# Performance work log

Hardware: AMD Instinct MI355X
Metric: run time of the kernel (lower is better)

The kernel has to match this reference:

```python
import jax, jax.numpy as jnp
import numpy as np

B, SQ, SK = 4, 4096, 1024
HID, SATD = 640, 768
NUM_HEADS, HEAD_DIM = 10, 64
GEO_RATIO, ROPE_BASE = 1.0, 10000.0
LOSS_W = 0.05


def _ln(x, g, b):
    m = x.mean(-1, keepdims=True)
    v = ((x - m) ** 2).mean(-1, keepdims=True)
    return (x - m) / jnp.sqrt(v + 1e-5) * g + b


def _rope(t, xy):
    # t: [B,H,S,D], xy: [B,S,2] continuous coordinates.
    # Half the rotary channels encode x, half encode y.
    q = HEAD_DIM // 4
    inv = ROPE_BASE ** (-jnp.arange(q, dtype=t.dtype) / q)  # [q]
    ang = jnp.concatenate([xy[..., 0:1] * GEO_RATIO * inv,
                           xy[..., 1:2] * GEO_RATIO * inv], axis=-1)  # [B,S,D/2]
    cos = jnp.cos(ang)[:, None]  # [B,1,S,D/2]
    sin = jnp.sin(ang)[:, None]
    t1, t2 = t[..., : HEAD_DIM // 2], t[..., HEAD_DIM // 2:]
    return jnp.concatenate([t1 * cos - t2 * sin, t1 * sin + t2 * cos], axis=-1)


def setup_inputs() -> dict:
    key = jax.random.key(0)
    ks = jax.random.split(key, 16)
    s = 0.02
    return {
        'hidden_states': jax.random.normal(ks[0], (B, SQ, HID), jnp.float32),
        'sat_tokens': jax.random.normal(ks[1], (B, SK, SATD), jnp.float32),
        'sat_xy': jax.random.normal(ks[2], (B, SK, 2), jnp.float32) * 10.0,
        'front_bev_xy': jax.random.normal(ks[3], (B, SQ, 2), jnp.float32) * 10.0,
        'front_plucker': jax.random.normal(ks[4], (B, SQ, 6), jnp.float32),
        'valid_mask': jax.random.uniform(ks[5], (B, SQ), jnp.float32),
        'Wq': jax.random.normal(ks[6], (HID, HID), jnp.float32) * s,
        'bq': jnp.zeros((HID,), jnp.float32),
        'sat_ln_g': jnp.ones((SATD,), jnp.float32),
        'sat_ln_b': jnp.zeros((SATD,), jnp.float32),
        'Wk': jax.random.normal(ks[7], (SATD, HID), jnp.float32) * s,
        'bk': jnp.zeros((HID,), jnp.float32),
        'Wv': jax.random.normal(ks[8], (SATD, HID), jnp.float32) * s,
        'bv': jnp.zeros((HID,), jnp.float32),
        'Wp1': jax.random.normal(ks[9], (6, HID), jnp.float32) * s,
        'bp1': jnp.zeros((HID,), jnp.float32),
        'Wp2': jax.random.normal(ks[10], (HID, HID), jnp.float32) * s,
        'bp2': jnp.zeros((HID,), jnp.float32),
        'gate_ln_g': jnp.ones((HID,), jnp.float32),
        'gate_ln_b': jnp.zeros((HID,), jnp.float32),
        'Wg': jax.random.normal(ks[11], (HID, 1), jnp.float32) * s,
        'bg': jnp.full((1,), -1.0, jnp.float32),
    }


def reference(hidden_states, sat_tokens, sat_xy, front_bev_xy, front_plucker,
              valid_mask, Wq, bq, sat_ln_g, sat_ln_b, Wk, bk, Wv, bv,
              Wp1, bp1, Wp2, bp2, gate_ln_g, gate_ln_b, Wg, bg):
    b = hidden_states.shape[0]
    sn = _ln(sat_tokens, sat_ln_g, sat_ln_b)
    query = hidden_states @ Wq + bq                      # [B,SQ,HID]
    key = sn @ Wk + bk                                   # [B,SK,HID]
    value = sn @ Wv + bv
    q = query.reshape(b, -1, NUM_HEADS, HEAD_DIM).transpose(0, 2, 1, 3)
    k = key.reshape(b, -1, NUM_HEADS, HEAD_DIM).transpose(0, 2, 1, 3)
    v = value.reshape(b, -1, NUM_HEADS, HEAD_DIM).transpose(0, 2, 1, 3)
    q = _rope(q, front_bev_xy)
    k = _rope(k, sat_xy)
    logits = jnp.einsum('bhqd,bhkd->bhqk', q, k) / np.sqrt(HEAD_DIM)
    probs = jax.nn.softmax(logits.astype(jnp.float32), axis=-1).astype(q.dtype)
    out_h = jnp.einsum('bhqk,bhkd->bhqd', probs, v)
    out_h = out_h.transpose(0, 2, 1, 3).reshape(b, -1, HID)
    # plucker-conditioned gate
    pf = jax.nn.silu(front_plucker @ Wp1 + bp1) @ Wp2 + bp2
    gate_ctx = hidden_states + pf
    gate = jax.nn.sigmoid(_ln(gate_ctx, gate_ln_g, gate_ln_b) @ Wg + bg)  # [B,SQ,1]
    vm = (valid_mask > 0.5)
    out = out_h * gate * vm[..., None].astype(out_h.dtype)
    # auxiliary masked-mean confidence loss over invalid positions
    inv = (~vm).astype(gate.dtype)
    denom = jnp.maximum(inv.sum(), 1.0)
    loss = (gate[..., 0] * inv).sum() / denom * LOSS_W
    return out, loss
```

## Files before the change

kernel.cpp:

```cpp
#include <hip/hip_runtime.h>
#include <cstdint>
#include <cstddef>

#define B_    4
#define SQ_   4096
#define SK_   1024
#define HID_  640
#define SATD_ 768
#define NH_   10
#define HD_   64

typedef __bf16 bf16_t;
typedef __bf16 bf16x4 __attribute__((ext_vector_type(4)));
typedef __bf16 bf16x8 __attribute__((ext_vector_type(8)));
typedef float  f32x4  __attribute__((ext_vector_type(4)));
typedef unsigned short u16x8 __attribute__((ext_vector_type(8)));

static __device__ __forceinline__ unsigned short f2u(float f) {
  bf16_t b = (bf16_t)f;
  return __builtin_bit_cast(unsigned short, b);
}
static __device__ __forceinline__ float u2f(unsigned short u) {
  return (float)__builtin_bit_cast(bf16_t, u);
}
static __device__ __forceinline__ f32x4 mfma16(bf16x8 a, bf16x8 b, f32x4 c) {
  return __builtin_amdgcn_mfma_f32_16x16x32_bf16(a, b, c, 0, 0, 0);
}
static __device__ __forceinline__ void glds16(const unsigned short* g, unsigned short* l) {
  __builtin_amdgcn_global_load_lds((const __attribute__((address_space(1))) void*)g,
                                   (__attribute__((address_space(3))) void*)l, 16, 0, 0);
}

__global__ __launch_bounds__(256) void k_transpose4(const float* __restrict__ Wq,
                                                    const float* __restrict__ Wk,
                                                    const float* __restrict__ Wv,
                                                    const float* __restrict__ Wp2,
                                                    unsigned short* __restrict__ wqT,
                                                    unsigned short* __restrict__ kvT,
                                                    unsigned short* __restrict__ wp2T) {
  __shared__ unsigned short tile[64 * 65];
  int seg = blockIdx.y;
  const float* W; unsigned short* D; int K;
  if (seg == 0)      { W = Wq;  D = wqT;  K = 640; }
  else if (seg == 1) { W = Wk;  D = kvT;  K = 768; }
  else if (seg == 2) { W = Wv;  D = kvT + (size_t)640 * 768; K = 768; }
  else               { W = Wp2; D = wp2T; K = 640; }
  const int ktiles = K / 64;
  int kt = blockIdx.x % ktiles, ntile = blockIdx.x / ktiles;
  if (ntile >= 10) return;
  const int k0 = kt * 64, n0 = ntile * 64;
  const int t = threadIdx.x, r = t >> 3, c8 = (t & 7) * 8;
#pragma unroll
  for (int i = 0; i < 2; i++) {
    int row = r + i * 32;
    const float* wp = W + (size_t)(k0 + row) * HID_ + n0 + c8;
    float4 a0 = *(const float4*)wp, a1 = *(const float4*)(wp + 4);
    tile[(c8 + 0) * 65 + row] = f2u(a0.x);
    tile[(c8 + 1) * 65 + row] = f2u(a0.y);
    tile[(c8 + 2) * 65 + row] = f2u(a0.z);
    tile[(c8 + 3) * 65 + row] = f2u(a0.w);
    tile[(c8 + 4) * 65 + row] = f2u(a1.x);
    tile[(c8 + 5) * 65 + row] = f2u(a1.y);
    tile[(c8 + 6) * 65 + row] = f2u(a1.z);
    tile[(c8 + 7) * 65 + row] = f2u(a1.w);
  }
  __syncthreads();
#pragma unroll
  for (int i = 0; i < 2; i++) {
    int nl = r + i * 32;
    u16x8 o;
#pragma unroll
    for (int u = 0; u < 8; u++) o[u] = tile[nl * 65 + c8 + u];
    *(u16x8*)(D + (size_t)(n0 + nl) * K + k0 + c8) = o;
  }
}

__global__ void k_concat_bias(const float* __restrict__ bk, const float* __restrict__ bv,
                              float* __restrict__ out) {
  int i = blockIdx.x * 256 + threadIdx.x;
  if (i < HID_) out[i] = bk[i];
  else if (i < 2 * HID_) out[i] = bv[i - HID_];
}

__global__ __launch_bounds__(256) void k_satln(const float* __restrict__ x,
                                               const float* __restrict__ g,
                                               const float* __restrict__ bta,
                                               unsigned short* __restrict__ out) {
  int r = blockIdx.x;
  const float* xr = x + (size_t)r * SATD_;
  int t = threadIdx.x;
  float v0 = xr[t], v1 = xr[t + 256], v2 = xr[t + 512];
  float s = v0 + v1 + v2;
  float ss = v0 * v0 + v1 * v1 + v2 * v2;
  __shared__ float sb[8];
  for (int o = 32; o; o >>= 1) { s += __shfl_xor(s, o); ss += __shfl_xor(ss, o); }
  if ((t & 63) == 0) { sb[t >> 6] = s; sb[4 + (t >> 6)] = ss; }
  __syncthreads();
  s  = sb[0] + sb[1] + sb[2] + sb[3];
  ss = sb[4] + sb[5] + sb[6] + sb[7];
  float m = s * (1.f / SATD_);
  float rstd = rsqrtf(ss * (1.f / SATD_) - m * m + 1e-5f);
  unsigned short* orow = out + (size_t)r * SATD_;
  orow[t]       = f2u((v0 - m) * rstd * g[t]       + bta[t]);
  orow[t + 256] = f2u((v1 - m) * rstd * g[t + 256] + bta[t + 256]);
  orow[t + 512] = f2u((v2 - m) * rstd * g[t + 512] + bta[t + 512]);
}

__global__ __launch_bounds__(256) void k_pf1(const float* __restrict__ plk,
                                             const float* __restrict__ W,
                                             const float* __restrict__ bias,
                                             unsigned short* __restrict__ out) {
  int i = blockIdx.x * 256 + threadIdx.x;
  int r = i / 80, c8 = (i - r * 80) * 8;
  const float* p = plk + (size_t)r * 6;
  float pv[6];
#pragma unroll
  for (int j = 0; j < 6; j++) pv[j] = p[j];
  u16x8 o;
#pragma unroll
  for (int u = 0; u < 8; u++) {
    int c = c8 + u;
    float a = bias[c];
#pragma unroll
    for (int j = 0; j < 6; j++) a += pv[j] * W[j * HID_ + c];
    o[u] = f2u(a / (1.f + __expf(-a)));
  }
  *(u16x8*)&out[(size_t)r * HID_ + c8] = o;
}

__global__ __launch_bounds__(256) void k_gemm_fused(const unsigned short* __restrict__ pf1,
                                                    const float* __restrict__ hidden,
                                                    const unsigned short* __restrict__ wp2T,
                                                    const unsigned short* __restrict__ wqT,
                                                    const float* __restrict__ bp2,
                                                    const float* __restrict__ bq,
                                                    unsigned short* __restrict__ pf2,
                                                    unsigned short* __restrict__ q_lin,
                                                    const float* __restrict__ bev_xy) {
  __shared__ unsigned short As[2][128 * 32];
  __shared__ unsigned short Bs[2][128 * 32];
  const int z = blockIdx.z;
  const int bx = blockIdx.x;
  const int xcd = bx & 7, jj = bx >> 3;
  const int bm = ((jj / 5) * 8 + xcd) * 128;
  const int bn = (jj % 5) * 128;
  const int K = 640, N = 640;
  const unsigned short* BT = z ? wqT : wp2T;
  const float* bias = z ? bq : bp2;
  unsigned short* C = z ? q_lin : pf2;

  const int t = threadIdx.x, wv = t >> 6, lane = t & 63;
  const int lc = lane & 15, quad = lane >> 4;
  const int wm = (wv >> 1) * 64, wn = (wv & 1) * 64;
  f32x4 acc[4][4];
  f32x4 zero = {0.f, 0.f, 0.f, 0.f};
#pragma unroll
  for (int i = 0; i < 4; i++)
#pragma unroll
    for (int j = 0; j < 4; j++) acc[i][j] = zero;
  const int srow = wv * 32 + (lane >> 2);
  const int sc8 = (lane & 3) * 8;

  for (int k0 = 0; k0 < K; k0 += 64) {
    __syncthreads();
    if (z == 0) {
#pragma unroll
      for (int h2 = 0; h2 < 2; h2++)
#pragma unroll
        for (int i = 0; i < 2; i++)
          glds16(pf1 + (size_t)(bm + srow + i * 16) * K + k0 + h2 * 32 + sc8,
                 &As[h2][(wv * 32 + i * 16) * 32]);
    } else {
      const int r4 = t >> 2, c4 = (t & 3) * 8;
#pragma unroll
      for (int h2 = 0; h2 < 2; h2++)
#pragma unroll
        for (int i = 0; i < 2; i++) {
          const float* ap = hidden + (size_t)(bm + r4 + i * 64) * K + k0 + h2 * 32 + c4;
          float4 a0 = *(const float4*)ap, a1 = *(const float4*)(ap + 4);
          u16x8 u = { f2u(a0.x), f2u(a0.y), f2u(a0.z), f2u(a0.w),
                      f2u(a1.x), f2u(a1.y), f2u(a1.z), f2u(a1.w) };
          *(u16x8*)&As[h2][(r4 + i * 64) * 32 + c4] = u;
        }
    }
#pragma unroll
    for (int h2 = 0; h2 < 2; h2++)
#pragma unroll
      for (int i = 0; i < 2; i++)
        glds16(BT + (size_t)(bn + srow + i * 16) * K + k0 + h2 * 32 + sc8,
               &Bs[h2][(wv * 32 + i * 16) * 32]);
    __syncthreads();
#pragma unroll
    for (int h2 = 0; h2 < 2; h2++) {
      bf16x8 af[4], bfr[4];
#pragma unroll
      for (int mt = 0; mt < 4; mt++) af[mt]  = *(const bf16x8*)&As[h2][(wm + mt * 16 + lc) * 32 + quad * 8];
#pragma unroll
      for (int nt = 0; nt < 4; nt++) bfr[nt] = *(const bf16x8*)&Bs[h2][(wn + nt * 16 + lc) * 32 + quad * 8];
#pragma unroll
      for (int mt = 0; mt < 4; mt++)
#pragma unroll
        for (int nt = 0; nt < 4; nt++) acc[mt][nt] = mfma16(af[mt], bfr[nt], acc[mt][nt]);
    }
  }

  float bsv[4];
#pragma unroll
  for (int nt = 0; nt < 4; nt++) bsv[nt] = bias[bn + wn + nt * 16 + lc];
  const float inv = __builtin_amdgcn_exp2f(-(float)lc * 0.8304820237218407f);
  const float qscale = 0.18033688011112042f;

#pragma unroll
  for (int mt = 0; mt < 4; mt++) {
    int row = bm + wm + mt * 16 + quad * 4;
#pragma unroll
    for (int r = 0; r < 4; r++) {
      unsigned short* crow = C + (size_t)(row + r) * N + bn + wn + lc;
      float v0 = acc[mt][0][r] + bsv[0];
      float v1 = acc[mt][1][r] + bsv[1];
      float v2 = acc[mt][2][r] + bsv[2];
      float v3 = acc[mt][3][r] + bsv[3];
      if (z) {
        float2 xy = *(const float2*)&bev_xy[(size_t)(row + r) * 2];
        float s0, c0, s1, c1;
        __sincosf(xy.x * inv, &s0, &c0);
        __sincosf(xy.y * inv, &s1, &c1);
        float n0 = (v0 * c0 - v2 * s0) * qscale;
        float n2 = (v0 * s0 + v2 * c0) * qscale;
        float n1 = (v1 * c1 - v3 * s1) * qscale;
        float n3 = (v1 * s1 + v3 * c1) * qscale;
        v0 = n0; v1 = n1; v2 = n2; v3 = n3;
      }
      crow[0]  = f2u(v0);
      crow[16] = f2u(v1);
      crow[32] = f2u(v2);
      crow[48] = f2u(v3);
    }
  }
}

__global__ __launch_bounds__(256) void k_gemm_kv(const unsigned short* __restrict__ sn,
                                                 const unsigned short* __restrict__ kvT,
                                                 const float* __restrict__ bias_kv,
                                                 unsigned short* __restrict__ k_lin,
                                                 unsigned short* __restrict__ vT,
                                                 const float* __restrict__ sat_xy) {
  __shared__ unsigned short As[2][128 * 32];
  __shared__ unsigned short Bs[2][128 * 32];
  const int bx = blockIdx.x;
  const int xcd = bx & 7, jj = bx >> 3;
  const int bm = ((jj / 10) * 8 + xcd) * 128;
  const int bn = (jj % 10) * 128;
  const int K = 768;
  const int t = threadIdx.x, wv = t >> 6, lane = t & 63;
  const int lc = lane & 15, quad = lane >> 4;
  const int wm = (wv >> 1) * 64, wn = (wv & 1) * 64;
  f32x4 acc[4][4];
  f32x4 zero = {0.f, 0.f, 0.f, 0.f};
#pragma unroll
  for (int i = 0; i < 4; i++)
#pragma unroll
    for (int j = 0; j < 4; j++) acc[i][j] = zero;
  const int srow = wv * 32 + (lane >> 2);
  const int sc8 = (lane & 3) * 8;

  for (int k0 = 0; k0 < K; k0 += 64) {
    __syncthreads();
#pragma unroll
    for (int h2 = 0; h2 < 2; h2++)
#pragma unroll
      for (int i = 0; i < 2; i++) {
        glds16(sn  + (size_t)(bm + srow + i * 16) * K + k0 + h2 * 32 + sc8,
               &As[h2][(wv * 32 + i * 16) * 32]);
        glds16(kvT + (size_t)(bn + srow + i * 16) * K + k0 + h2 * 32 + sc8,
               &Bs[h2][(wv * 32 + i * 16) * 32]);
      }
    __syncthreads();
#pragma unroll
    for (int h2 = 0; h2 < 2; h2++) {
      bf16x8 af[4], bfr[4];
#pragma unroll
      for (int mt = 0; mt < 4; mt++) af[mt]  = *(const bf16x8*)&As[h2][(wm + mt * 16 + lc) * 32 + quad * 8];
#pragma unroll
      for (int nt = 0; nt < 4; nt++) bfr[nt] = *(const bf16x8*)&Bs[h2][(wn + nt * 16 + lc) * 32 + quad * 8];
#pragma unroll
      for (int mt = 0; mt < 4; mt++)
#pragma unroll
        for (int nt = 0; nt < 4; nt++) acc[mt][nt] = mfma16(af[mt], bfr[nt], acc[mt][nt]);
    }
  }

  float bsv[4];
#pragma unroll
  for (int nt = 0; nt < 4; nt++) bsv[nt] = bias_kv[bn + wn + nt * 16 + lc];
  const bool isV = (bn >= HID_);
  const float inv = __builtin_amdgcn_exp2f(-(float)lc * 0.8304820237218407f);

  if (!isV) {
#pragma unroll
    for (int mt = 0; mt < 4; mt++) {
      int row = bm + wm + mt * 16 + quad * 4;
#pragma unroll
      for (int r = 0; r < 4; r++) {
        unsigned short* crow = k_lin + (size_t)(row + r) * HID_ + bn + wn + lc;
        float v0 = acc[mt][0][r] + bsv[0];
        float v1 = acc[mt][1][r] + bsv[1];
        float v2 = acc[mt][2][r] + bsv[2];
        float v3 = acc[mt][3][r] + bsv[3];
        float2 xy = *(const float2*)&sat_xy[(size_t)(row + r) * 2];
        float s0, c0, s1, c1;
        __sincosf(xy.x * inv, &s0, &c0);
        __sincosf(xy.y * inv, &s1, &c1);
        crow[0]  = f2u(v0 * c0 - v2 * s0);
        crow[32] = f2u(v0 * s0 + v2 * c0);
        crow[16] = f2u(v1 * c1 - v3 * s1);
        crow[48] = f2u(v1 * s1 + v3 * c1);
      }
    }
  } else {
#pragma unroll
    for (int mt = 0; mt < 4; mt++) {
      int row0 = bm + wm + mt * 16 + quad * 4;
      int bidx = row0 >> 10, key0 = row0 & 1023;
#pragma unroll
      for (int nt = 0; nt < 4; nt++) {
        int d = bn - HID_ + wn + nt * 16 + lc;
        bf16x4 v;
#pragma unroll
        for (int r = 0; r < 4; r++) v[r] = (bf16_t)(acc[mt][nt][r] + bsv[nt]);
        *(bf16x4*)(vT + ((size_t)(bidx * HID_ + d) << 10) + key0) = v;
      }
    }
  }
}

__global__ __launch_bounds__(256) void k_gate(const float* __restrict__ hid,
                                              const unsigned short* __restrict__ pf2,
                                              const float* __restrict__ g,
                                              const float* __restrict__ be,
                                              const float* __restrict__ Wg,
                                              const float* __restrict__ bg,
                                              const float* __restrict__ vm,
                                              float* __restrict__ gate_buf,
                                              float* __restrict__ lg_buf) {
  int r = blockIdx.x;
  const float* hr = hid + (size_t)r * HID_;
  const unsigned short* pr = pf2 + (size_t)r * HID_;
  int t = threadIdx.x;
  __shared__ float xb[HID_];
  __shared__ float sb[8];
  float s = 0.f, ss = 0.f;
  for (int c = t; c < HID_; c += 256) {
    float x = hr[c] + u2f(pr[c]);
    xb[c] = x; s += x; ss += x * x;
  }
  for (int o = 32; o; o >>= 1) { s += __shfl_xor(s, o); ss += __shfl_xor(ss, o); }
  if ((t & 63) == 0) { sb[t >> 6] = s; sb[4 + (t >> 6)] = ss; }
  __syncthreads();
  s  = sb[0] + sb[1] + sb[2] + sb[3];
  ss = sb[4] + sb[5] + sb[6] + sb[7];
  float m = s * (1.f / HID_);
  float rstd = rsqrtf(ss * (1.f / HID_) - m * m + 1e-5f);
  float dacc = 0.f;
  for (int c = t; c < HID_; c += 256)
    dacc += ((xb[c] - m) * rstd * g[c] + be[c]) * Wg[c];
  for (int o = 32; o; o >>= 1) dacc += __shfl_xor(dacc, o);
  __syncthreads();
  if ((t & 63) == 0) sb[t >> 6] = dacc;
  __syncthreads();
  if (t == 0) {
    float dsum = sb[0] + sb[1] + sb[2] + sb[3] + bg[0];
    float gate = 1.f / (1.f + __expf(-dsum));
    float v = vm[r];
    gate_buf[r] = (v > 0.5f) ? gate : 0.f;
    lg_buf[r]   = (v > 0.5f) ? 0.f : gate;
  }
}

__global__ __launch_bounds__(256) void k_attn(const unsigned short* __restrict__ q_lin,
                                              const unsigned short* __restrict__ k_lin,
                                              const unsigned short* __restrict__ vT,
                                              const float* __restrict__ gate_buf,
                                              float* __restrict__ out) {
  __shared__ unsigned short Ks[64 * 72];
  __shared__ unsigned short Vt[64 * 72];
  __shared__ unsigned short Pt[4][32 * 72];
  const int qb = blockIdx.x * 128;
  const int bh = blockIdx.y;
  const int b = bh / NH_, h = bh - b * NH_;
  const int t = threadIdx.x, wv = t >> 6, lane = t & 63;
  const int lc = lane & 15, quad = lane >> 4;
  unsigned short* myPt = &Pt[wv][0];

  const unsigned short* qbase = q_lin + (size_t)(b * SQ_ + qb + wv * 32 + lc) * HID_ + h * HD_;
  bf16x8 qf[2][2];
#pragma unroll
  for (int g = 0; g < 2; g++) {
    qf[g][0] = *(const bf16x8*)(qbase + (size_t)g * 16 * HID_ + quad * 8);
    qf[g][1] = *(const bf16x8*)(qbase + (size_t)g * 16 * HID_ + 32 + quad * 8);
  }
  f32x4 zero = {0.f, 0.f, 0.f, 0.f};
  f32x4 O[2][4];
#pragma unroll
  for (int g = 0; g < 2; g++)
#pragma unroll
    for (int dt = 0; dt < 4; dt++) O[g][dt] = zero;
  float l_run[2] = {0.f, 0.f};

  const unsigned short* Kg = k_lin + (size_t)b * SK_ * HID_ + h * HD_;
  const unsigned short* Vg = vT + ((size_t)b * HID_ + h * HD_) * SK_;
  const int srow = t >> 3, scol = (t & 7) * 8;

  for (int kc = 0; kc < SK_; kc += 64) {
    __syncthreads();
#pragma unroll
    for (int i = 0; i < 2; i++) {
      int row = srow + i * 32;
      *(u16x8*)&Ks[row * 72 + scol] = *(const u16x8*)(Kg + (size_t)(kc + row) * HID_ + scol);
      *(u16x8*)&Vt[row * 72 + scol] = *(const u16x8*)(Vg + (size_t)row * SK_ + kc + scol);
    }
    __syncthreads();

    f32x4 ST[2][4];
#pragma unroll
    for (int kt = 0; kt < 4; kt++) {
      bf16x8 ka0 = *(const bf16x8*)&Ks[(kt * 16 + lc) * 72 + quad * 8];
      bf16x8 ka1 = *(const bf16x8*)&Ks[(kt * 16 + lc) * 72 + 32 + quad * 8];
#pragma unroll
      for (int g = 0; g < 2; g++)
        ST[g][kt] = mfma16(ka1, qf[g][1], mfma16(ka0, qf[g][0], zero));
    }
#pragma unroll
    for (int g = 0; g < 2; g++) {
      float rs = 0.f;
#pragma unroll
      for (int kt = 0; kt < 4; kt++) {
        bf16x4 pk;
#pragma unroll
        for (int r = 0; r < 4; r++) {
          float p = __builtin_amdgcn_exp2f(ST[g][kt][r]);
          rs += p;
          pk[r] = (bf16_t)p;
        }
        *(bf16x4*)&myPt[(g * 16 + lc) * 72 + kt * 16 + quad * 4] = pk;
      }
      rs += __shfl_xor(rs, 16);
      rs += __shfl_xor(rs, 32);
      l_run[g] += rs;
    }
#pragma unroll
    for (int ks = 0; ks < 2; ks++) {
      bf16x8 va[4];
#pragma unroll
      for (int dt = 0; dt < 4; dt++)
        va[dt] = *(const bf16x8*)&Vt[(dt * 16 + lc) * 72 + ks * 32 + quad * 8];
#pragma unroll
      for (int g = 0; g < 2; g++) {
        bf16x8 pb = *(const bf16x8*)&myPt[(g * 16 + lc) * 72 + ks * 32 + quad * 8];
#pragma unroll
        for (int dt = 0; dt < 4; dt++)
          O[g][dt] = mfma16(va[dt], pb, O[g][dt]);
      }
    }
  }

#pragma unroll
  for (int g = 0; g < 2; g++) {
    int rg = b * SQ_ + qb + wv * 32 + g * 16 + lc;
    float gv = gate_buf[rg] / l_run[g];
    float* orow = out + (size_t)rg * HID_ + h * HD_;
#pragma unroll
    for (int dt = 0; dt < 4; dt++) {
      f32x4 o4 = O[g][dt] * gv;
      *(f32x4*)&orow[dt * 16 + quad * 4] = o4;
    }
  }
}

__global__ __launch_bounds__(256) void k_loss(const float* __restrict__ lg,
                                              const float* __restrict__ vm,
                                              float* __restrict__ out_loss) {
  int t = threadIdx.x;
  float s = 0.f, cnt = 0.f;
  for (int i = t; i < B_ * SQ_; i += 256) {
    s += lg[i];
    cnt += (vm[i] > 0.5f) ? 0.f : 1.f;
  }
  __shared__ float sb[8];
  for (int o = 32; o; o >>= 1) { s += __shfl_xor(s, o); cnt += __shfl_xor(cnt, o); }
  if ((t & 63) == 0) { sb[t >> 6] = s; sb[4 + (t >> 6)] = cnt; }
  __syncthreads();
  if (t == 0) {
    s   = sb[0] + sb[1] + sb[2] + sb[3];
    cnt = sb[4] + sb[5] + sb[6] + sb[7];
    out_loss[0] = s / fmaxf(cnt, 1.f) * 0.05f;
  }
}

extern "C" void kernel_launch(void* const* d_in, const int* in_sizes, int n_in,
                              void* d_out, int out_size, void* d_ws, size_t ws_size,
                              hipStream_t stream) {
  (void)in_sizes; (void)n_in; (void)out_size; (void)ws_size;
  const float* hidden = (const float*)d_in[0];
  const float* sat    = (const float*)d_in[1];
  const float* sat_xy = (const float*)d_in[2];
  const float* bev_xy = (const float*)d_in[3];
  const float* plk    = (const float*)d_in[4];
  const float* vm     = (const float*)d_in[5];
  const float* Wq     = (const float*)d_in[6];
  const float* bq     = (const float*)d_in[7];
  const float* slg    = (const float*)d_in[8];
  const float* slb    = (const float*)d_in[9];
  const float* Wk     = (const float*)d_in[10];
  const float* bk     = (const float*)d_in[11];
  const float* Wv     = (const float*)d_in[12];
  const float* bv     = (const float*)d_in[13];
  const float* Wp1    = (const float*)d_in[14];
  const float* bp1    = (const float*)d_in[15];
  const float* Wp2    = (const float*)d_in[16];
  const float* bp2    = (const float*)d_in[17];
  const float* glg    = (const float*)d_in[18];
  const float* glb    = (const float*)d_in[19];
  const float* Wg     = (const float*)d_in[20];
  const float* bg     = (const float*)d_in[21];
  float* out = (float*)d_out;

  char* ws = (char*)d_ws;
  size_t off = 0;
  auto alloc = [&](size_t bytes) -> char* {
    char* p = ws + off;
    off += (bytes + 255) & ~(size_t)255;
    return p;
  };
  char* regP = alloc((size_t)16384 * 640 * 2);
  unsigned short* pf1   = (unsigned short*)regP;
  unsigned short* k_lin = (unsigned short*)regP;
  unsigned short* vT    = (unsigned short*)(regP + (size_t)4096 * 640 * 2);
  unsigned short* pf2   = (unsigned short*)alloc((size_t)16384 * 640 * 2);
  unsigned short* q_lin = (unsigned short*)alloc((size_t)16384 * 640 * 2);
  unsigned short* sn    = (unsigned short*)alloc((size_t)4096 * 768 * 2);
  unsigned short* wqT   = (unsigned short*)alloc((size_t)640 * 640 * 2);
  unsigned short* kvT   = (unsigned short*)alloc((size_t)1280 * 768 * 2);
  unsigned short* wp2T  = (unsigned short*)alloc((size_t)640 * 640 * 2);
  float* bias_kv  = (float*)alloc(1280 * 4);
  float* gate_buf = (float*)alloc(16384 * 4);
  float* lg_buf   = (float*)alloc(16384 * 4);

  {
    dim3 g(120, 4);
    k_transpose4<<<g, 256, 0, stream>>>(Wq, Wk, Wv, Wp2, wqT, kvT, wp2T);
  }
  k_concat_bias<<<5, 256, 0, stream>>>(bk, bv, bias_kv);

  k_pf1<<<16384 * 80 / 256, 256, 0, stream>>>(plk, Wp1, bp1, pf1);
  k_satln<<<4096, 256, 0, stream>>>(sat, slg, slb, sn);

  {
    dim3 g(640, 1, 2);
    k_gemm_fused<<<g, 256, 0, stream>>>(pf1, hidden, wp2T, wqT, bp2, bq, pf2, q_lin, bev_xy);
  }
  k_gemm_kv<<<320, 256, 0, stream>>>(sn, kvT, bias_kv, k_lin, vT, sat_xy);

  k_gate<<<16384, 256, 0, stream>>>(hidden, pf2, glg, glb, Wg, bg, vm, gate_buf, lg_buf);

  {
    dim3 g(SQ_ / 128, B_ * NH_);
    k_attn<<<g, 256, 0, stream>>>(q_lin, k_lin, vT, gate_buf, out);
  }
  k_loss<<<1, 256, 0, stream>>>(lg_buf, vm, out + (size_t)B_ * SQ_ * HID_);
}
```

Before: 354.3 us.

## Merge prep kernels, fuse KV GEMM into batched GEMM, warp-per-row gate, prefetch attn tiles

Folds the weight transpose, bias concat, satellite LayerNorm and plucker MLP first layer into one launch, and runs the K/V projection as a third z-slice of the Q/pf2 GEMM kernel. The gate kernel now handles one row per wavefront, which removes shared-memory reductions and block barriers. The attention kernel prefetches the next K/V chunk into registers while computing on the current one. pf2 is stored in the output buffer as scratch, and the workspace regions are no longer aliased. The aim is to cut launch overhead and idle tails and to overlap global loads with compute, at the cost of higher register pressure in attention.

New measurement: 309.1 us. 1.15x faster.

```diff
diff --git a/kernel.cpp b/kernel.cpp
--- a/kernel.cpp
+++ b/kernel.cpp
@@ -31,123 +31,140 @@
                                    (__attribute__((address_space(3))) void*)l, 16, 0, 0);
 }
 
-__global__ __launch_bounds__(256) void k_transpose4(const float* __restrict__ Wq,
-                                                    const float* __restrict__ Wk,
-                                                    const float* __restrict__ Wv,
-                                                    const float* __restrict__ Wp2,
-                                                    unsigned short* __restrict__ wqT,
-                                                    unsigned short* __restrict__ kvT,
-                                                    unsigned short* __restrict__ wp2T) {
+__global__ __launch_bounds__(256) void k_prep(const float* __restrict__ Wq,
+                                              const float* __restrict__ Wk,
+                                              const float* __restrict__ Wv,
+                                              const float* __restrict__ Wp2,
+                                              unsigned short* __restrict__ wqT,
+                                              unsigned short* __restrict__ kvT,
+                                              unsigned short* __restrict__ wp2T,
+                                              const float* __restrict__ bk,
+                                              const float* __restrict__ bv,
+                                              float* __restrict__ bias_kv,
+                                              const float* __restrict__ sat,
+                                              const float* __restrict__ slg,
+                                              const float* __restrict__ slb,
+                                              unsigned short* __restrict__ sn,
+                                              const float* __restrict__ plk,
+                                              const float* __restrict__ Wp1,
+                                              const float* __restrict__ bp1,
+                                              unsigned short* __restrict__ pf1) {
   __shared__ unsigned short tile[64 * 65];
-  int seg = blockIdx.y;
-  const float* W; unsigned short* D; int K;
-  if (seg == 0)      { W = Wq;  D = wqT;  K = 640; }
-  else if (seg == 1) { W = Wk;  D = kvT;  K = 768; }
-  else if (seg == 2) { W = Wv;  D = kvT + (size_t)640 * 768; K = 768; }
-  else               { W = Wp2; D = wp2T; K = 640; }
-  const int ktiles = K / 64;
-  int kt = blockIdx.x % ktiles, ntile = blockIdx.x / ktiles;
-  if (ntile >= 10) return;
-  const int k0 = kt * 64, n0 = ntile * 64;
-  const int t = threadIdx.x, r = t >> 3, c8 = (t & 7) * 8;
-#pragma unroll
-  for (int i = 0; i < 2; i++) {
-    int row = r + i * 32;
-    const float* wp = W + (size_t)(k0 + row) * HID_ + n0 + c8;
-    float4 a0 = *(const float4*)wp, a1 = *(const float4*)(wp + 4);
-    tile[(c8 + 0) * 65 + row] = f2u(a0.x);
-    tile[(c8 + 1) * 65 + row] = f2u(a0.y);
-    tile[(c8 + 2) * 65 + row] = f2u(a0.z);
-    tile[(c8 + 3) * 65 + row] = f2u(a0.w);
-    tile[(c8 + 4) * 65 + row] = f2u(a1.x);
-    tile[(c8 + 5) * 65 + row] = f2u(a1.y);
-    tile[(c8 + 6) * 65 + row] = f2u(a1.z);
-    tile[(c8 + 7) * 65 + row] = f2u(a1.w);
-  }
-  __syncthreads();
-#pragma unroll
-  for (int i = 0; i < 2; i++) {
-    int nl = r + i * 32;
+  __shared__ float sb[8];
+  const int bx = blockIdx.x, t = threadIdx.x;
+
+  if (bx < 480) {
+    int seg = bx / 120, inner = bx % 120;
+    const float* W; unsigned short* D; int K;
+    if (seg == 0)      { W = Wq;  D = wqT;  K = 640; }
+    else if (seg == 1) { W = Wk;  D = kvT;  K = 768; }
+    else if (seg == 2) { W = Wv;  D = kvT + (size_t)640 * 768; K = 768; }
+    else               { W = Wp2; D = wp2T; K = 640; }
+    const int ktiles = K / 64;
+    int kt = inner % ktiles, ntile = inner / ktiles;
+    if (ntile >= 10) return;
+    const int k0 = kt * 64, n0 = ntile * 64;
+    const int r = t >> 3, c8 = (t & 7) * 8;
+#pragma unroll
+    for (int i = 0; i < 2; i++) {
+      int row = r + i * 32;
+      const float* wp = W + (size_t)(k0 + row) * HID_ + n0 + c8;
+      float4 a0 = *(const float4*)wp, a1 = *(const float4*)(wp + 4);
+      tile[(c8 + 0) * 65 + row] = f2u(a0.x);
+      tile[(c8 + 1) * 65 + row] = f2u(a0.y);
+      tile[(c8 + 2) * 65 + row] = f2u(a0.z);
+      tile[(c8 + 3) * 65 + row] = f2u(a0.w);
+      tile[(c8 + 4) * 65 + row] = f2u(a1.x);
+      tile[(c8 + 5) * 65 + row] = f2u(a1.y);
+      tile[(c8 + 6) * 65 + row] = f2u(a1.z);
+      tile[(c8 + 7) * 65 + row] = f2u(a1.w);
+    }
+    __syncthreads();
+#pragma unroll
+    for (int i = 0; i < 2; i++) {
+      int nl = r + i * 32;
+      u16x8 o;
+#pragma unroll
+      for (int u = 0; u < 8; u++) o[u] = tile[nl * 65 + c8 + u];
+      *(u16x8*)(D + (size_t)(n0 + nl) * K + k0 + c8) = o;
+    }
+  } else if (bx < 485) {
+    int i = (bx - 480) * 256 + t;
+    if (i < HID_) bias_kv[i] = bk[i];
+    else if (i < 2 * HID_) bias_kv[i] = bv[i - HID_];
+  } else if (bx < 4581) {
+    int r = bx - 485;
+    const float* xr = sat + (size_t)r * SATD_;
+    float v0 = xr[t], v1 = xr[t + 256], v2 = xr[t + 512];
+    float s = v0 + v1 + v2;
+    float ss = v0 * v0 + v1 * v1 + v2 * v2;
+    for (int o = 32; o; o >>= 1) { s += __shfl_xor(s, o); ss += __shfl_xor(ss, o); }
+    if ((t & 63) == 0) { sb[t >> 6] = s; sb[4 + (t >> 6)] = ss; }
+    __syncthreads();
+    s  = sb[0] + sb[1] + sb[2] + sb[3];
+    ss = sb[4] + sb[5] + sb[6] + sb[7];
+    float m = s * (1.f / SATD_);
+    float rstd = rsqrtf(ss * (1.f / SATD_) - m * m + 1e-5f);
+    unsigned short* orow = sn + (size_t)r * SATD_;
+    orow[t]       = f2u((v0 - m) * rstd * slg[t]       + slb[t]);
+    orow[t + 256] = f2u((v1 - m) * rstd * slg[t + 256] + slb[t + 256]);
+    orow[t + 512] = f2u((v2 - m) * rstd * slg[t + 512] + slb[t + 512]);
+  } else {
+    int i = (bx - 4581) * 256 + t;
+    int r = i / 80, c8 = (i - r * 80) * 8;
+    const float* p = plk + (size_t)r * 6;
+    float pv[6];
+#pragma unroll
+    for (int j = 0; j < 6; j++) pv[j] = p[j];
     u16x8 o;
 #pragma unroll
-    for (int u = 0; u < 8; u++) o[u] = tile[nl * 65 + c8 + u];
-    *(u16x8*)(D + (size_t)(n0 + nl) * K + k0 + c8) = o;
-  }
-}
-
-__global__ void k_concat_bias(const float* __restrict__ bk, const float* __restrict__ bv,
-                              float* __restrict__ out) {
-  int i = blockIdx.x * 256 + threadIdx.x;
-  if (i < HID_) out[i] = bk[i];
-  else if (i < 2 * HID_) out[i] = bv[i - HID_];
-}
-
-__global__ __launch_bounds__(256) void k_satln(const float* __restrict__ x,
-                                               const float* __restrict__ g,
-                                               const float* __restrict__ bta,
-                                               unsigned short* __restrict__ out) {
-  int r = blockIdx.x;
-  const float* xr = x + (size_t)r * SATD_;
-  int t = threadIdx.x;
-  float v0 = xr[t], v1 = xr[t + 256], v2 = xr[t + 512];
-  float s = v0 + v1 + v2;
-  float ss = v0 * v0 + v1 * v1 + v2 * v2;
-  __shared__ float sb[8];
-  for (int o = 32; o; o >>= 1) { s += __shfl_xor(s, o); ss += __shfl_xor(ss, o); }
-  if ((t & 63) == 0) { sb[t >> 6] = s; sb[4 + (t >> 6)] = ss; }
-  __syncthreads();
-  s  = sb[0] + sb[1] + sb[2] + sb[3];
-  ss = sb[4] + sb[5] + sb[6] + sb[7];
-  float m = s * (1.f / SATD_);
-  float rstd = rsqrtf(ss * (1.f / SATD_) - m * m + 1e-5f);
-  unsigned short* orow = out + (size_t)r * SATD_;
-  orow[t]       = f2u((v0 - m) * rstd * g[t]       + bta[t]);
-  orow[t + 256] = f2u((v1 - m) * rstd * g[t + 256] + bta[t + 256]);
-  orow[t + 512] = f2u((v2 - m) * rstd * g[t + 512] + bta[t + 512]);
-}
-
-__global__ __launch_bounds__(256) void k_pf1(const float* __restrict__ plk,
-                                             const float* __restrict__ W,
-                                             const float* __restrict__ bias,
-                                             unsigned short* __restrict__ out) {
-  int i = blockIdx.x * 256 + threadIdx.x;
-  int r = i / 80, c8 = (i - r * 80) * 8;
-  const float* p = plk + (size_t)r * 6;
-  float pv[6];
-#pragma unroll
-  for (int j = 0; j < 6; j++) pv[j] = p[j];
-  u16x8 o;
-#pragma unroll
-  for (int u = 0; u < 8; u++) {
-    int c = c8 + u;
-    float a = bias[c];
-#pragma unroll
-    for (int j = 0; j < 6; j++) a += pv[j] * W[j * HID_ + c];
-    o[u] = f2u(a / (1.f + __expf(-a)));
-  }
-  *(u16x8*)&out[(size_t)r * HID_ + c8] = o;
-}
-
-__global__ __launch_bounds__(256) void k_gemm_fused(const unsigned short* __restrict__ pf1,
-                                                    const float* __restrict__ hidden,
-                                                    const unsigned short* __restrict__ wp2T,
-                                                    const unsigned short* __restrict__ wqT,
-                                                    const float* __restrict__ bp2,
-                                                    const float* __restrict__ bq,
-                                                    unsigned short* __restrict__ pf2,
-                                                    unsigned short* __restrict__ q_lin,
-                                                    const float* __restrict__ bev_xy) {
+    for (int u = 0; u < 8; u++) {
+      int c = c8 + u;
+      float a = bp1[c];
+#pragma unroll
+      for (int j = 0; j < 6; j++) a += pv[j] * Wp1[j * HID_ + c];
+      o[u] = f2u(a / (1.f + __expf(-a)));
+    }
+    *(u16x8*)&pf1[(size_t)r * HID_ + c8] = o;
+  }
+}
+
+__global__ __launch_bounds__(256) void k_gemm3(const unsigned short* __restrict__ pf1,
+                                               const float* __restrict__ hidden,
+                                               const unsigned short* __restrict__ sn,
+                                               const unsigned short* __restrict__ wp2T,
+                                               const unsigned short* __restrict__ wqT,
+                                               const unsigned short* __restrict__ kvT,
+                                               const float* __restrict__ bp2,
+                                               const float* __restrict__ bq,
+                                               const float* __restrict__ bias_kv,
+                                               unsigned short* __restrict__ pf2,
+                                               unsigned short* __restrict__ q_lin,
+                                               unsigned short* __restrict__ k_lin,
+                                               unsigned short* __restrict__ vT,
+                                               const float* __restrict__ bev_xy,
+                                               const float* __restrict__ sat_xy) {
   __shared__ unsigned short As[2][128 * 32];
   __shared__ unsigned short Bs[2][128 * 32];
   const int z = blockIdx.z;
   const int bx = blockIdx.x;
-  const int xcd = bx & 7, jj = bx >> 3;
-  const int bm = ((jj / 5) * 8 + xcd) * 128;
-  const int bn = (jj % 5) * 128;
-  const int K = 640, N = 640;
-  const unsigned short* BT = z ? wqT : wp2T;
-  const float* bias = z ? bq : bp2;
-  unsigned short* C = z ? q_lin : pf2;
+  int bm, bn, K;
+  const unsigned short* BT;
+  const float* bias;
+  if (z == 2) {
+    if (bx >= 320) return;
+    const int xcd = bx & 7, jj = bx >> 3;
+    bm = ((jj / 10) * 8 + xcd) * 128;
+    bn = (jj % 10) * 128;
+    K = 768; BT = kvT; bias = bias_kv;
+  } else {
+    const int xcd = bx & 7, jj = bx >> 3;
+    bm = ((jj / 5) * 8 + xcd) * 128;
+    bn = (jj % 5) * 128;
+    K = 640;
+    BT = z ? wqT : wp2T;
+    bias = z ? bq : bp2;
+  }
 
   const int t = threadIdx.x, wv = t >> 6, lane = t & 63;
   const int lc = lane & 15, quad = lane >> 4;
@@ -169,6 +186,13 @@
 #pragma unroll
         for (int i = 0; i < 2; i++)
           glds16(pf1 + (size_t)(bm + srow + i * 16) * K + k0 + h2 * 32 + sc8,
+                 &As[h2][(wv * 32 + i * 16) * 32]);
+    } else if (z == 2) {
+#pragma unroll
+      for (int h2 = 0; h2 < 2; h2++)
+#pragma unroll
+        for (int i = 0; i < 2; i++)
+          glds16(sn + (size_t)(bm + srow + i * 16) * K + k0 + h2 * 32 + sc8,
                  &As[h2][(wv * 32 + i * 16) * 32]);
     } else {
       const int r4 = t >> 2, c4 = (t & 3) * 8;
@@ -208,95 +232,43 @@
 #pragma unroll
   for (int nt = 0; nt < 4; nt++) bsv[nt] = bias[bn + wn + nt * 16 + lc];
   const float inv = __builtin_amdgcn_exp2f(-(float)lc * 0.8304820237218407f);
-  const float qscale = 0.18033688011112042f;
-
-#pragma unroll
-  for (int mt = 0; mt < 4; mt++) {
-    int row = bm + wm + mt * 16 + quad * 4;
-#pragma unroll
-    for (int r = 0; r < 4; r++) {
-      unsigned short* crow = C + (size_t)(row + r) * N + bn + wn + lc;
-      float v0 = acc[mt][0][r] + bsv[0];
-      float v1 = acc[mt][1][r] + bsv[1];
-      float v2 = acc[mt][2][r] + bsv[2];
-      float v3 = acc[mt][3][r] + bsv[3];
-      if (z) {
+
+  if (z == 0) {
+#pragma unroll
+    for (int mt = 0; mt < 4; mt++) {
+      int row = bm + wm + mt * 16 + quad * 4;
+#pragma unroll
+      for (int r = 0; r < 4; r++) {
+        unsigned short* crow = pf2 + (size_t)(row + r) * HID_ + bn + wn + lc;
+        crow[0]  = f2u(acc[mt][0][r] + bsv[0]);
+        crow[16] = f2u(acc[mt][1][r] + bsv[1]);
+        crow[32] = f2u(acc[mt][2][r] + bsv[2]);
+        crow[48] = f2u(acc[mt][3][r] + bsv[3]);
+      }
+    }
+  } else if (z == 1) {
+    const float qscale = 0.18033688011112042f;
+#pragma unroll
+    for (int mt = 0; mt < 4; mt++) {
+      int row = bm + wm + mt * 16 + quad * 4;
+#pragma unroll
+      for (int r = 0; r < 4; r++) {
+        unsigned short* crow = q_lin + (size_t)(row + r) * HID_ + bn + wn + lc;
+        float v0 = acc[mt][0][r] + bsv[0];
+        float v1 = acc[mt][1][r] + bsv[1];
+        float v2 = acc[mt][2][r] + bsv[2];
+        float v3 = acc[mt][3][r] + bsv[3];
         float2 xy = *(const float2*)&bev_xy[(size_t)(row + r) * 2];
         float s0, c0, s1, c1;
         __sincosf(xy.x * inv, &s0, &c0);
         __sincosf(xy.y * inv, &s1, &c1);
-        float n0 = (v0 * c0 - v2 * s0) * qscale;
-        float n2 = (v0 * s0 + v2 * c0) * qscale;
-        float n1 = (v1 * c1 - v3 * s1) * qscale;
-        float n3 = (v1 * s1 + v3 * c1) * qscale;
-        v0 = n0; v1 = n1; v2 = n2; v3 = n3;
-      }
-      crow[0]  = f2u(v0);
-      crow[16] = f2u(v1);
-      crow[32] = f2u(v2);
-      crow[48] = f2u(v3);
-    }
-  }
-}
-
-__global__ __launch_bounds__(256) void k_gemm_kv(const unsigned short* __restrict__ sn,
-                                                 const unsigned short* __restrict__ kvT,
-                                                 const float* __restrict__ bias_kv,
-                                                 unsigned short* __restrict__ k_lin,
-                                                 unsigned short* __restrict__ vT,
-                                                 const float* __restrict__ sat_xy) {
-  __shared__ unsigned short As[2][128 * 32];
-  __shared__ unsigned short Bs[2][128 * 32];
-  const int bx = blockIdx.x;
-  const int xcd = bx & 7, jj = bx >> 3;
-  const int bm = ((jj / 10) * 8 + xcd) * 128;
-  const int bn = (jj % 10) * 128;
-  const int K = 768;
-  const int t = threadIdx.x, wv = t >> 6, lane = t & 63;
-  const int lc = lane & 15, quad = lane >> 4;
-  const int wm = (wv >> 1) * 64, wn = (wv & 1) * 64;
-  f32x4 acc[4][4];
-  f32x4 zero = {0.f, 0.f, 0.f, 0.f};
-#pragma unroll
-  for (int i = 0; i < 4; i++)
-#pragma unroll
-    for (int j = 0; j < 4; j++) acc[i][j] = zero;
-  const int srow = wv * 32 + (lane >> 2);
-  const int sc8 = (lane & 3) * 8;
-
-  for (int k0 = 0; k0 < K; k0 += 64) {
-    __syncthreads();
-#pragma unroll
-    for (int h2 = 0; h2 < 2; h2++)
-#pragma unroll
-      for (int i = 0; i < 2; i++) {
-        glds16(sn  + (size_t)(bm + srow + i * 16) * K + k0 + h2 * 32 + sc8,
-               &As[h2][(wv * 32 + i * 16) * 32]);
-        glds16(kvT + (size_t)(bn + srow + i * 16) * K + k0 + h2 * 32 + sc8,
-               &Bs[h2][(wv * 32 + i * 16) * 32]);
-      }
-    __syncthreads();
-#pragma unroll
-    for (int h2 = 0; h2 < 2; h2++) {
-      bf16x8 af[4], bfr[4];
-#pragma unroll
-      for (int mt = 0; mt < 4; mt++) af[mt]  = *(const bf16x8*)&As[h2][(wm + mt * 16 + lc) * 32 + quad * 8];
-#pragma unroll
-      for (int nt = 0; nt < 4; nt++) bfr[nt] = *(const bf16x8*)&Bs[h2][(wn + nt * 16 + lc) * 32 + quad * 8];
-#pragma unroll
-      for (int mt = 0; mt < 4; mt++)
-#pragma unroll
-        for (int nt = 0; nt < 4; nt++) acc[mt][nt] = mfma16(af[mt], bfr[nt], acc[mt][nt]);
-    }
-  }
-
-  float bsv[4];
-#pragma unroll
-  for (int nt = 0; nt < 4; nt++) bsv[nt] = bias_kv[bn + wn + nt * 16 + lc];
-  const bool isV = (bn >= HID_);
-  const float inv = __builtin_amdgcn_exp2f(-(float)lc * 0.8304820237218407f);
-
-  if (!isV) {
+        crow[0]  = f2u((v0 * c0 - v2 * s0) * qscale);
+        crow[32] = f2u((v0 * s0 + v2 * c0) * qscale);
+        crow[16] = f2u((v1 * c1 - v3 * s1) * qscale);
+        crow[48] = f2u((v1 * s1 + v3 * c1) * qscale);
+      }
+    }
+  } else if (bn < HID_) {
 #pragma unroll
     for (int mt = 0; mt < 4; mt++) {
       int row = bm + wm + mt * 16 + quad * 4;
@@ -343,37 +315,35 @@
                                               const float* __restrict__ vm,
                                               float* __restrict__ gate_buf,
                                               float* __restrict__ lg_buf) {
-  int r = blockIdx.x;
-  const float* hr = hid + (size_t)r * HID_;
-  const unsigned short* pr = pf2 + (size_t)r * HID_;
-  int t = threadIdx.x;
-  __shared__ float xb[HID_];
-  __shared__ float sb[8];
+  const int row = blockIdx.x * 4 + (threadIdx.x >> 6);
+  const int lane = threadIdx.x & 63;
+  const float* hr = hid + (size_t)row * HID_;
+  const unsigned short* pr = pf2 + (size_t)row * HID_;
+  float x[10];
   float s = 0.f, ss = 0.f;
-  for (int c = t; c < HID_; c += 256) {
-    float x = hr[c] + u2f(pr[c]);
-    xb[c] = x; s += x; ss += x * x;
-  }
+#pragma unroll
+  for (int u = 0; u < 10; u++) {
+    int c = u * 64 + lane;
+    float v = hr[c] + u2f(pr[c]);
+    x[u] = v; s += v; ss += v * v;
+  }
+#pragma unroll
   for (int o = 32; o; o >>= 1) { s += __shfl_xor(s, o); ss += __shfl_xor(ss, o); }
-  if ((t & 63) == 0) { sb[t >> 6] = s; sb[4 + (t >> 6)] = ss; }
-  __syncthreads();
-  s  = sb[0] + sb[1] + sb[2] + sb[3];
-  ss = sb[4] + sb[5] + sb[6] + sb[7];
   float m = s * (1.f / HID_);
   float rstd = rsqrtf(ss * (1.f / HID_) - m * m + 1e-5f);
-  float dacc = 0.f;
-  for (int c = t; c < HID_; c += 256)
-    dacc += ((xb[c] - m) * rstd * g[c] + be[c]) * Wg[c];
-  for (int o = 32; o; o >>= 1) dacc += __shfl_xor(dacc, o);
-  __syncthreads();
-  if ((t & 63) == 0) sb[t >> 6] = dacc;
-  __syncthreads();
-  if (t == 0) {
-    float dsum = sb[0] + sb[1] + sb[2] + sb[3] + bg[0];
-    float gate = 1.f / (1.f + __expf(-dsum));
-    float v = vm[r];
-    gate_buf[r] = (v > 0.5f) ? gate : 0.f;
-    lg_buf[r]   = (v > 0.5f) ? 0.f : gate;
+  float d = 0.f;
+#pragma unroll
+  for (int u = 0; u < 10; u++) {
+    int c = u * 64 + lane;
+    d += ((x[u] - m) * rstd * g[c] + be[c]) * Wg[c];
+  }
+#pragma unroll
+  for (int o = 32; o; o >>= 1) d += __shfl_xor(d, o);
+  if (lane == 0) {
+    float gate = 1.f / (1.f + __expf(-(d + bg[0])));
+    float v = vm[row];
+    gate_buf[row] = (v > 0.5f) ? gate : 0.f;
+    lg_buf[row]   = (v > 0.5f) ? 0.f : gate;
   }
 }
 
@@ -411,15 +381,29 @@
   const unsigned short* Vg = vT + ((size_t)b * HID_ + h * HD_) * SK_;
   const int srow = t >> 3, scol = (t & 7) * 8;
 
+  u16x8 kpre[2], vpre[2];
+#pragma unroll
+  for (int i = 0; i < 2; i++) {
+    kpre[i] = *(const u16x8*)(Kg + (size_t)(srow + i * 32) * HID_ + scol);
+    vpre[i] = *(const u16x8*)(Vg + (size_t)(srow + i * 32) * SK_ + scol);
+  }
+
   for (int kc = 0; kc < SK_; kc += 64) {
     __syncthreads();
 #pragma unroll
     for (int i = 0; i < 2; i++) {
       int row = srow + i * 32;
-      *(u16x8*)&Ks[row * 72 + scol] = *(const u16x8*)(Kg + (size_t)(kc + row) * HID_ + scol);
-      *(u16x8*)&Vt[row * 72 + scol] = *(const u16x8*)(Vg + (size_t)row * SK_ + kc + scol);
+      *(u16x8*)&Ks[row * 72 + scol] = kpre[i];
+      *(u16x8*)&Vt[row * 72 + scol] = vpre[i];
     }
     __syncthreads();
+    if (kc + 64 < SK_) {
+#pragma unroll
+      for (int i = 0; i < 2; i++) {
+        kpre[i] = *(const u16x8*)(Kg + (size_t)(kc + 64 + srow + i * 32) * HID_ + scol);
+        vpre[i] = *(const u16x8*)(Vg + (size_t)(srow + i * 32) * SK_ + kc + 64 + scol);
+      }
+    }
 
     f32x4 ST[2][4];
 #pragma unroll
@@ -532,12 +516,11 @@
     off += (bytes + 255) & ~(size_t)255;
     return p;
   };
-  char* regP = alloc((size_t)16384 * 640 * 2);
-  unsigned short* pf1   = (unsigned short*)regP;
-  unsigned short* k_lin = (unsigned short*)regP;
-  unsigned short* vT    = (unsigned short*)(regP + (size_t)4096 * 640 * 2);
-  unsigned short* pf2   = (unsigned short*)alloc((size_t)16384 * 640 * 2);
+  unsigned short* pf2   = (unsigned short*)d_out;
+  unsigned short* pf1   = (unsigned short*)alloc((size_t)16384 * 640 * 2);
   unsigned short* q_lin = (unsigned short*)alloc((size_t)16384 * 640 * 2);
+  unsigned short* k_lin = (unsigned short*)alloc((size_t)4096 * 640 * 2);
+  unsigned short* vT    = (unsigned short*)alloc((size_t)B_ * HID_ * SK_ * 2);
   unsigned short* sn    = (unsigned short*)alloc((size_t)4096 * 768 * 2);
   unsigned short* wqT   = (unsigned short*)alloc((size_t)640 * 640 * 2);
   unsigned short* kvT   = (unsigned short*)alloc((size_t)1280 * 768 * 2);
@@ -546,22 +529,19 @@
   float* gate_buf = (float*)alloc(16384 * 4);
   float* lg_buf   = (float*)alloc(16384 * 4);
 
+  k_prep<<<9701, 256, 0, stream>>>(Wq, Wk, Wv, Wp2, wqT, kvT, wp2T,
+                                   bk, bv, bias_kv,
+                                   sat, slg, slb, sn,
+                                   plk, Wp1, bp1, pf1);
+
   {
-    dim3 g(120, 4);
-    k_transpose4<<<g, 256, 0, stream>>>(Wq, Wk, Wv, Wp2, wqT, kvT, wp2T);
-  }
-  k_concat_bias<<<5, 256, 0, stream>>>(bk, bv, bias_kv);
-
-  k_pf1<<<16384 * 80 / 256, 256, 0, stream>>>(plk, Wp1, bp1, pf1);
-  k_satln<<<4096, 256, 0, stream>>>(sat, slg, slb, sn);
-
-  {
-    dim3 g(640, 1, 2);
-    k_gemm_fused<<<g, 256, 0, stream>>>(pf1, hidden, wp2T, wqT, bp2, bq, pf2, q_lin, bev_xy);
-  }
-  k_gemm_kv<<<320, 256, 0, stream>>>(sn, kvT, bias_kv, k_lin, vT, sat_xy);
-
-  k_gate<<<16384, 256, 0, stream>>>(hidden, pf2, glg, glb, Wg, bg, vm, gate_buf, lg_buf);
+    dim3 g(640, 1, 3);
+    k_gemm3<<<g, 256, 0, stream>>>(pf1, hidden, sn, wp2T, wqT, kvT,
+                                   bp2, bq, bias_kv,
+                                   pf2, q_lin, k_lin, vT, bev_xy, sat_xy);
+  }
+
+  k_gate<<<4096, 256, 0, stream>>>(hidden, pf2, glg, glb, Wg, bg, vm, gate_buf, lg_buf);
 
   {
     dim3 g(SQ_ / 128, B_ * NH_);
```
